# Optimization experiments

Hardware: AMD Instinct MI355X
Metric: run time of the kernel (lower is better)

The kernel has to match this reference:

```python
import jax, jax.numpy as jnp
import numpy as np

NUM_HEADS = 16
EPS = 1e-5


def _layernorm(x, w):
    # torch LayerNorm (biased variance), bias=False
    m = jnp.mean(x, axis=-1, keepdims=True)
    v = jnp.mean(jnp.square(x - m), axis=-1, keepdims=True)
    return (x - m) * jax.lax.rsqrt(v + EPS) * w


def setup_inputs() -> dict:
    key = jax.random.key(0)
    ks = jax.random.split(key, 8)
    B, S, H, A = 2, 2048, 1024, 1024
    hd = H // NUM_HEADS
    return {
        "x": jax.random.normal(ks[0], (B, S, H), jnp.float32),
        "ada_cond": jax.random.normal(ks[1], (B, A), jnp.float32),
        "freqs": jax.random.normal(ks[2], (S, hd // 2, 2), jnp.float32),
        "w_qkv": jax.random.normal(ks[3], (3 * H, H), jnp.float32) * (1.0 / np.sqrt(H)),
        "w_o": jax.random.normal(ks[4], (H, H), jnp.float32) * (1.0 / np.sqrt(H)),
        "ln_w": jnp.ones((H,), jnp.float32),
        "mod_w": jax.random.normal(ks[5], (3 * H, A), jnp.float32) * 0.02,
        "mod_b": jax.random.normal(ks[6], (3 * H,), jnp.float32) * 0.02,
        "qn_w": jnp.ones((hd,), jnp.float32),
        "kn_w": jnp.ones((hd,), jnp.float32),
    }


def reference(x, ada_cond, freqs, w_qkv, w_o, ln_w, mod_w, mod_b, qn_w, kn_w):
    B, S, H = x.shape
    nh = NUM_HEADS
    hd = H // nh

    # pre-norm + AdaLN modulation (with gate)
    h = _layernorm(x, ln_w)
    mod = (jax.nn.silu(ada_cond) @ mod_w.T + mod_b)[:, None, :]  # [B,1,3H]
    scale, shift, gate = jnp.split(mod, 3, axis=-1)
    h = h * (scale + 1.0) + shift

    # QKV projection and head split
    qkv = h @ w_qkv.T                                  # [B,S,3H]
    q, k, v = jnp.split(qkv, 3, axis=-1)
    to_heads = lambda t: t.reshape(B, S, nh, hd).transpose(0, 2, 1, 3)  # [B,nh,S,hd]
    q, k, v = to_heads(q), to_heads(k), to_heads(v)

    # per-head QK layernorm
    q = _layernorm(q, qn_w)
    k = _layernorm(k, kn_w)

    # RoPE (complex rotation via interleaved pairs)
    f = freqs[:S].reshape(1, 1, S, hd // 2, 2)

    def rope(t):
        tr = t.reshape(B, nh, S, hd // 2, 2)
        re = tr[..., 0] * f[..., 0] - tr[..., 1] * f[..., 1]
        im = tr[..., 1] * f[..., 0] + tr[..., 0] * f[..., 1]
        return jnp.stack([re, im], axis=-1).reshape(B, nh, S, hd)

    q, k = rope(q), rope(k)

    # scaled dot-product attention (non-causal)
    scores = jnp.einsum("bhqd,bhkd->bhqk", q, k) * (1.0 / np.sqrt(hd))
    attn = jax.nn.softmax(scores, axis=-1)
    o = jnp.einsum("bhqk,bhkd->bhqd", attn, v)
    o = o.transpose(0, 2, 1, 3).reshape(B, S, H)

    return (o @ w_o.T) * gate
```

## Files before the change

### kernel.cpp

```cpp
#include <hip/hip_runtime.h>
#include <hip/hip_bf16.h>
#include <hip/hip_fp16.h>
#include <math.h>

#define B_ 2
#define S_ 2048
#define H_ 1024
#define A_ 1024
#define NH_ 16
#define HD_ 64
#define H3_ 3072
#define EPS_ 1e-5f

typedef __attribute__((ext_vector_type(8))) short short8;
typedef __attribute__((ext_vector_type(4))) float floatx4;
typedef __attribute__((ext_vector_type(4))) _Float16 half4v;
typedef __attribute__((ext_vector_type(2))) __fp16 fp16x2;

__device__ inline unsigned short f2bf(float x) {
    union { float f; unsigned u; } v; v.f = x;
    unsigned r = v.u + 0x7fffu + ((v.u >> 16) & 1u);
    return (unsigned short)(r >> 16);
}

__device__ inline unsigned pk_bf16(float a, float b) {
    union { __hip_bfloat162 h; unsigned u; } v;
    v.h = __float22bfloat162_rn(make_float2(a, b));
    return v.u;
}

__device__ inline unsigned pk_f16(float a, float b) {
    union { __half2 h; unsigned u; } v;
    v.h = __float22half2_rn(make_float2(a, b));
    return v.u;
}

__device__ inline void gld_lds16(const void* g, void* l) {
    __builtin_amdgcn_global_load_lds(
        (const __attribute__((address_space(1))) unsigned int*)g,
        (__attribute__((address_space(3))) unsigned int*)l, 16, 0, 0);
}


__global__ __launch_bounds__(256) void cast_bf16_kernel(
    const float* __restrict__ in, unsigned short* __restrict__ out, int n)
{
    int i = (blockIdx.x * 256 + threadIdx.x) * 8;
    if (i >= n) return;
    float4 a = *(const float4*)(in + i);
    float4 b = *(const float4*)(in + i + 4);
    uint4 o;
    o.x = pk_bf16(a.x, a.y);
    o.y = pk_bf16(a.z, a.w);
    o.z = pk_bf16(b.x, b.y);
    o.w = pk_bf16(b.z, b.w);
    *(uint4*)(out + i) = o;
}

__global__ __launch_bounds__(256) void mod_gemv_kernel(
    const float* __restrict__ ada, const float* __restrict__ mod_w,
    const float* __restrict__ mod_b, float* __restrict__ mod)
{
    int wid = threadIdx.x >> 6;
    int lane = threadIdx.x & 63;
    int idx = blockIdx.x * 4 + wid;
    int b = idx / H3_;
    int j = idx % H3_;
    const float* ar = ada + (size_t)b * A_;
    const float* wr = mod_w + (size_t)j * A_;
    float acc = 0.f;
    for (int a = lane; a < A_; a += 64) {
        float av = ar[a];
        float sv = av / (1.f + __expf(-av));
        acc += sv * wr[a];
    }
    #pragma unroll
    for (int m = 1; m < 64; m <<= 1) acc += __shfl_xor(acc, m);
    if (lane == 0) mod[idx] = acc + mod_b[j];
}

__global__ __launch_bounds__(256) void ln_mod_kernel(
    const float* __restrict__ x, const float* __restrict__ ln_w,
    const float* __restrict__ mod, unsigned short* __restrict__ hout)
{
    int row = blockIdx.x;
    int b = row >> 11;
    const float* xr = x + (size_t)row * H_;
    int t = threadIdx.x;
    float4 xv = *(const float4*)(xr + t * 4);
    float s1 = xv.x + xv.y + xv.z + xv.w;
    float s2 = xv.x*xv.x + xv.y*xv.y + xv.z*xv.z + xv.w*xv.w;
    #pragma unroll
    for (int m = 1; m < 64; m <<= 1) { s1 += __shfl_xor(s1, m); s2 += __shfl_xor(s2, m); }
    __shared__ float r1[4], r2[4];
    int wid = t >> 6, lane = t & 63;
    if (lane == 0) { r1[wid] = s1; r2[wid] = s2; }
    __syncthreads();
    s1 = r1[0] + r1[1] + r1[2] + r1[3];
    s2 = r2[0] + r2[1] + r2[2] + r2[3];
    float mean = s1 * (1.f / H_);
    float var  = s2 * (1.f / H_) - mean * mean;
    float rstd = rsqrtf(var + EPS_);
    const float* mrow = mod + (size_t)b * H3_;
    float4 wv = *(const float4*)(ln_w + t * 4);
    float4 sc = *(const float4*)(mrow + t * 4);
    float4 sh = *(const float4*)(mrow + H_ + t * 4);
    float4 hv;
    hv.x = (xv.x - mean) * rstd * wv.x * (sc.x + 1.f) + sh.x;
    hv.y = (xv.y - mean) * rstd * wv.y * (sc.y + 1.f) + sh.y;
    hv.z = (xv.z - mean) * rstd * wv.z * (sc.z + 1.f) + sh.z;
    hv.w = (xv.w - mean) * rstd * wv.w * (sc.w + 1.f) + sh.w;
    uint2 o;
    o.x = pk_bf16(hv.x, hv.y);
    o.y = pk_bf16(hv.z, hv.w);
    *(uint2*)(hout + (size_t)row * H_ + t * 4) = o;
}

__global__ __launch_bounds__(256) void gemm_qkv_fused_kernel(
    const unsigned short* __restrict__ A, const unsigned short* __restrict__ Bm,
    const float* __restrict__ freqs, const float* __restrict__ qn_w,
    const float* __restrict__ kn_w, unsigned short* __restrict__ qout,
    unsigned short* __restrict__ kout, unsigned short* __restrict__ vtout)
{
    __shared__ unsigned short As[2][128 * 32];
    __shared__ unsigned short Bs[2][128 * 32];
    const int K = H_;
    int t = threadIdx.x;
    int w = t >> 6, lane = t & 63;
    int q16 = lane & 15, quad = lane >> 4;
    int wm = w >> 1, wn = w & 1;
    int m0 = blockIdx.y * 128, n0 = blockIdx.x * 128;

    int srow = 2 * (lane >> 3) + ((lane >> 2) & 1);
    int scol = ((lane & 3) ^ ((lane >> 3) & 3)) << 3;
    const unsigned short* ga = A + (size_t)(m0 + (w << 5) + srow) * K + scol;
    const unsigned short* gb = Bm + (size_t)(n0 + (w << 5) + srow) * K + scol;
    int ldst0 = (w * 16) * 64;
    int ldst1 = (w * 16 + 8) * 64;

    floatx4 acc[4][4];
    #pragma unroll
    for (int mt = 0; mt < 4; ++mt)
        #pragma unroll
        for (int nt = 0; nt < 4; ++nt)
            acc[mt][nt] = (floatx4){0.f, 0.f, 0.f, 0.f};

    int abase = (wm * 32 + (q16 >> 1)) * 64 + (q16 & 1) * 32
              + ((quad ^ ((q16 >> 1) & 3)) << 3);
    int bbase = (wn * 32 + (q16 >> 1)) * 64 + (q16 & 1) * 32
              + ((quad ^ ((q16 >> 1) & 3)) << 3);

    gld_lds16(ga, &As[0][ldst0]);
    gld_lds16(ga + (size_t)16 * K, &As[0][ldst1]);
    gld_lds16(gb, &Bs[0][ldst0]);
    gld_lds16(gb + (size_t)16 * K, &Bs[0][ldst1]);
    __syncthreads();

    int cur = 0;
    for (int kt = 0; kt < K / 32; ++kt) {
        const unsigned short* curA = &As[cur][0];
        const unsigned short* curB = &Bs[cur][0];
        short8 af[4], bf[4];
        #pragma unroll
        for (int mt = 0; mt < 4; ++mt)
            af[mt] = *(const short8*)&curA[abase + mt * 512];
        #pragma unroll
        for (int nt = 0; nt < 4; ++nt)
            bf[nt] = *(const short8*)&curB[bbase + nt * 512];

        if (kt + 1 < K / 32) {
            const unsigned short* ga2 = ga + (kt + 1) * 32;
            const unsigned short* gb2 = gb + (kt + 1) * 32;
            int nb = cur ^ 1;
            gld_lds16(ga2, &As[nb][ldst0]);
            gld_lds16(ga2 + (size_t)16 * K, &As[nb][ldst1]);
            gld_lds16(gb2, &Bs[nb][ldst0]);
            gld_lds16(gb2 + (size_t)16 * K, &Bs[nb][ldst1]);
        }

        #pragma unroll
        for (int mt = 0; mt < 4; ++mt)
            #pragma unroll
            for (int nt = 0; nt < 4; ++nt)
                acc[mt][nt] = __builtin_amdgcn_mfma_f32_16x16x32_bf16(
                    af[mt], bf[nt], acc[mt][nt], 0, 0, 0);

        __syncthreads();
        cur ^= 1;
    }

    int n_base = n0 + wn * 64;
    int sec = n_base >> 10;
    int head = (n_base & 1023) >> 6;

    if (sec == 2) {
        #pragma unroll
        for (int mt = 0; mt < 4; ++mt) {
            int m = m0 + wm * 64 + mt * 16 + quad * 4;
            int b = m >> 11, s = m & (S_ - 1);
            #pragma unroll
            for (int nt = 0; nt < 4; ++nt) {
                int d = nt * 16 + q16;
                unsigned short* dst =
                    vtout + ((size_t)((b * 16 + head) * 64 + d)) * S_ + s;
                uint2 pk;
                pk.x = pk_f16(acc[mt][nt][0], acc[mt][nt][1]);
                pk.y = pk_f16(acc[mt][nt][2], acc[mt][nt][3]);
                *(uint2*)dst = pk;
            }
        }
    } else {
        const float* nw = (sec == 0) ? qn_w : kn_w;
        float w4[4];
        #pragma unroll
        for (int nt = 0; nt < 4; ++nt) w4[nt] = nw[nt * 16 + q16];
        unsigned short* outp = (sec == 0) ? qout : kout;
        float qscale = (sec == 0) ? 0.1803368801111244f : 1.0f;

        #pragma unroll
        for (int mt = 0; mt < 4; ++mt) {
            #pragma unroll
            for (int i = 0; i < 4; ++i) {
                int m = m0 + wm * 64 + mt * 16 + quad * 4 + i;
                int b = m >> 11, s = m & (S_ - 1);
                float v0 = acc[mt][0][i], v1 = acc[mt][1][i];
                float v2 = acc[mt][2][i], v3 = acc[mt][3][i];
                float s1 = (v0 + v1) + (v2 + v3);
                float s2 = (v0 * v0 + v1 * v1) + (v2 * v2 + v3 * v3);
                #pragma unroll
                for (int msk = 1; msk < 16; msk <<= 1) {
                    s1 += __shfl_xor(s1, msk);
                    s2 += __shfl_xor(s2, msk);
                }
                float mean = s1 * (1.f / 64);
                float var  = s2 * (1.f / 64) - mean * mean;
                float rstd = rsqrtf(var + EPS_);
                float vv[4];
                vv[0] = (v0 - mean) * rstd * w4[0];
                vv[1] = (v1 - mean) * rstd * w4[1];
                vv[2] = (v2 - mean) * rstd * w4[2];
                vv[3] = (v3 - mean) * rstd * w4[3];
                const float* fr = freqs + (size_t)s * 64;
                unsigned short* orow = outp + ((size_t)((b * 16 + head) * S_ + s)) * 64;
                #pragma unroll
                for (int nt = 0; nt < 4; ++nt) {
                    int c = nt * 16 + q16;
                    float vp = __shfl_xor(vv[nt], 1);
                    float2 ff = *(const float2*)(fr + (c & ~1));
                    float r = (c & 1) ? (vv[nt] * ff.x + vp * ff.y)
                                      : (vv[nt] * ff.x - vp * ff.y);
                    orow[c] = f2bf(r * qscale);
                }
            }
        }
    }
}

__global__ __launch_bounds__(256) void gemm_bt_bf16_kernel(
    const unsigned short* __restrict__ A, const unsigned short* __restrict__ Bm,
    float* __restrict__ C, int M, int N, int K,
    const float* __restrict__ gate, int gate_stride, int batch_shift)
{
    __shared__ unsigned short As[2][128 * 32];
    __shared__ unsigned short Bs[2][64 * 32];
    int t = threadIdx.x;
    int w = t >> 6, lane = t & 63;
    int q16 = lane & 15, quad = lane >> 4;
    int m0 = blockIdx.y * 128, n0 = blockIdx.x * 64;

    int srow = 2 * (lane >> 3) + ((lane >> 2) & 1);
    int scol = ((lane & 3) ^ ((lane >> 3) & 3)) << 3;
    const unsigned short* ga = A + (size_t)(m0 + (w << 5) + srow) * K + scol;
    const unsigned short* gb = Bm + (size_t)(n0 + (w << 4) + srow) * K + scol;
    int ldstA0 = (w * 16) * 64;
    int ldstA1 = (w * 16 + 8) * 64;
    int ldstB  = (w * 8) * 64;

    floatx4 acc[2][4];
    #pragma unroll
    for (int mt = 0; mt < 2; ++mt)
        #pragma unroll
        for (int nt = 0; nt < 4; ++nt)
            acc[mt][nt] = (floatx4){0.f, 0.f, 0.f, 0.f};

    int abase = (w * 16 + (q16 >> 1)) * 64 + (q16 & 1) * 32
              + ((quad ^ ((q16 >> 1) & 3)) << 3);
    int bbase = (q16 >> 1) * 64 + (q16 & 1) * 32
              + ((quad ^ ((q16 >> 1) & 3)) << 3);

    gld_lds16(ga, &As[0][ldstA0]);
    gld_lds16(ga + (size_t)16 * K, &As[0][ldstA1]);
    gld_lds16(gb, &Bs[0][ldstB]);
    __syncthreads();

    int cur = 0;
    for (int kt = 0; kt < K / 32; ++kt) {
        const unsigned short* curA = &As[cur][0];
        const unsigned short* curB = &Bs[cur][0];
        short8 af[2], bf[4];
        #pragma unroll
        for (int mt = 0; mt < 2; ++mt)
            af[mt] = *(const short8*)&curA[abase + mt * 512];
        #pragma unroll
        for (int nt = 0; nt < 4; ++nt)
            bf[nt] = *(const short8*)&curB[bbase + nt * 512];

        if (kt + 1 < K / 32) {
            const unsigned short* ga2 = ga + (kt + 1) * 32;
            const unsigned short* gb2 = gb + (kt + 1) * 32;
            int nb = cur ^ 1;
            gld_lds16(ga2, &As[nb][ldstA0]);
            gld_lds16(ga2 + (size_t)16 * K, &As[nb][ldstA1]);
            gld_lds16(gb2, &Bs[nb][ldstB]);
        }

        #pragma unroll
        for (int mt = 0; mt < 2; ++mt)
            #pragma unroll
            for (int nt = 0; nt < 4; ++nt)
                acc[mt][nt] = __builtin_amdgcn_mfma_f32_16x16x32_bf16(
                    af[mt], bf[nt], acc[mt][nt], 0, 0, 0);

        __syncthreads();
        cur ^= 1;
    }

    #pragma unroll
    for (int mt = 0; mt < 2; ++mt) {
        #pragma unroll
        for (int i = 0; i < 4; ++i) {
            int m = m0 + w * 32 + mt * 16 + quad * 4 + i;
            float* crow = C + (size_t)m * N;
            const float* grow = gate ? gate + (size_t)(m >> batch_shift) * gate_stride
                                     : nullptr;
            #pragma unroll
            for (int nt = 0; nt < 4; ++nt) {
                int n = n0 + nt * 16 + q16;
                float v = acc[mt][nt][i];
                if (gate) v *= grow[n];
                crow[n] = v;
            }
        }
    }
}

__global__ __launch_bounds__(256, 2) void attn_mfma_kernel(
    const unsigned short* __restrict__ q, const unsigned short* __restrict__ k,
    const unsigned short* __restrict__ vt, unsigned short* __restrict__ o)
{
    __shared__ __align__(16) float obuf[4096];
    __shared__ float lbuf[4][4][16];

    int t = threadIdx.x;
    int w = t >> 6, lane = t & 63;
    int q16 = lane & 15, quad = lane >> 4;
    int bh = blockIdx.y, b = bh >> 4, h = bh & 15;
    int s0 = blockIdx.x * 64;

    const unsigned short* qgp = q + ((size_t)bh * S_ + s0) * HD_;
    short8 qf[4][2];
    #pragma unroll
    for (int qg = 0; qg < 4; ++qg)
        #pragma unroll
        for (int hh = 0; hh < 2; ++hh)
            qf[qg][hh] = *(const short8*)(qgp + (16 * qg + q16) * HD_ + hh * 32 + quad * 8);

    const unsigned short* kg = k + (size_t)bh * S_ * HD_ + (16 * w + q16) * HD_ + quad * 8;
    const unsigned short* vg = vt + (size_t)bh * 64 * S_ + (size_t)q16 * S_
                             + 16 * w + quad * 4;

    short8 kf_nx0 = *(const short8*)kg;
    short8 kf_nx1 = *(const short8*)(kg + 32);
    half4v vf_nx[4];
    #pragma unroll
    for (int nd = 0; nd < 4; ++nd)
        vf_nx[nd] = *(const half4v*)(vg + nd * 16 * S_);

    union { half4v h; uint2 u; } ones;
    ones.u.x = 0x3C003C00u; ones.u.y = 0x3C003C00u;

    floatx4 acc_o[4][4];
    floatx4 acc_l[4];
    #pragma unroll
    for (int nd = 0; nd < 4; ++nd)
        #pragma unroll
        for (int qg = 0; qg < 4; ++qg)
            acc_o[nd][qg] = (floatx4){0.f, 0.f, 0.f, 0.f};
    #pragma unroll
    for (int qg = 0; qg < 4; ++qg) acc_l[qg] = (floatx4){0.f, 0.f, 0.f, 0.f};

    for (int kt = 0; kt < S_ / 64; ++kt) {
        short8 kf0 = kf_nx0, kf1 = kf_nx1;
        half4v vf0 = vf_nx[0], vf1 = vf_nx[1], vf2 = vf_nx[2], vf3 = vf_nx[3];

        if (kt + 1 < S_ / 64) {
            kg += 64 * HD_; vg += 64;
            kf_nx0 = *(const short8*)kg;
            kf_nx1 = *(const short8*)(kg + 32);
            #pragma unroll
            for (int nd = 0; nd < 4; ++nd)
                vf_nx[nd] = *(const half4v*)(vg + nd * 16 * S_);
        }

        floatx4 sc[4];
        #pragma unroll
        for (int qg = 0; qg < 4; ++qg) sc[qg] = (floatx4){-12.f, -12.f, -12.f, -12.f};
        #pragma unroll
        for (int qg = 0; qg < 4; ++qg) {
            sc[qg] = __builtin_amdgcn_mfma_f32_16x16x32_bf16(kf0, qf[qg][0], sc[qg], 0, 0, 0);
            sc[qg] = __builtin_amdgcn_mfma_f32_16x16x32_bf16(kf1, qf[qg][1], sc[qg], 0, 0, 0);
        }

        #pragma unroll
        for (int qg = 0; qg < 4; ++qg) {
            float p0 = __builtin_amdgcn_exp2f(sc[qg][0]);
            float p1 = __builtin_amdgcn_exp2f(sc[qg][1]);
            float p2 = __builtin_amdgcn_exp2f(sc[qg][2]);
            float p3 = __builtin_amdgcn_exp2f(sc[qg][3]);
            union { half4v h; fp16x2 f2[2]; } pf;
            pf.f2[0] = __builtin_amdgcn_cvt_pkrtz(p0, p1);
            pf.f2[1] = __builtin_amdgcn_cvt_pkrtz(p2, p3);
            acc_l[qg] = __builtin_amdgcn_mfma_f32_16x16x16f16(ones.h, pf.h, acc_l[qg], 0, 0, 0);
            acc_o[0][qg] = __builtin_amdgcn_mfma_f32_16x16x16f16(vf0, pf.h, acc_o[0][qg], 0, 0, 0);
            acc_o[1][qg] = __builtin_amdgcn_mfma_f32_16x16x16f16(vf1, pf.h, acc_o[1][qg], 0, 0, 0);
            acc_o[2][qg] = __builtin_amdgcn_mfma_f32_16x16x16f16(vf2, pf.h, acc_o[2][qg], 0, 0, 0);
            acc_o[3][qg] = __builtin_amdgcn_mfma_f32_16x16x16f16(vf3, pf.h, acc_o[3][qg], 0, 0, 0);
        }
    }

    if (quad == 0) {
        #pragma unroll
        for (int qg = 0; qg < 4; ++qg) lbuf[w][qg][q16] = acc_l[qg][0];
    }
    __syncthreads();
    float linv = 1.f / (lbuf[0][w][q16] + lbuf[1][w][q16] + lbuf[2][w][q16] + lbuf[3][w][q16]);

    float* myw = obuf + ((w * 4) * 64 + lane) * 4;
    float* myr = obuf + (w * 64 + lane) * 4;
    unsigned short* og = o + ((size_t)(b * S_ + s0 + 16 * w + q16)) * H_ + h * HD_ + 4 * quad;

    #pragma unroll
    for (int nd = 0; nd < 4; ++nd) {
        __syncthreads();
        #pragma unroll
        for (int qg = 0; qg < 4; ++qg)
            *(floatx4*)(myw + qg * 256) = acc_o[nd][qg];
        __syncthreads();
        floatx4 r0 = *(const floatx4*)(myr);
        floatx4 r1 = *(const floatx4*)(myr + 1024);
        floatx4 r2 = *(const floatx4*)(myr + 2048);
        floatx4 r3 = *(const floatx4*)(myr + 3072);
        floatx4 s = (r0 + r1) + (r2 + r3);
        uint2 pk;
        pk.x = pk_bf16(s[0] * linv, s[1] * linv);
        pk.y = pk_bf16(s[2] * linv, s[3] * linv);
        *(uint2*)(og + nd * 16) = pk;
    }
}

extern "C" void kernel_launch(void* const* d_in, const int* in_sizes, int n_in,
                              void* d_out, int out_size, void* d_ws, size_t ws_size,
                              hipStream_t stream)
{
    const float* x     = (const float*)d_in[0];
    const float* ada   = (const float*)d_in[1];
    const float* freqs = (const float*)d_in[2];
    const float* w_qkv = (const float*)d_in[3];
    const float* w_o   = (const float*)d_in[4];
    const float* ln_w  = (const float*)d_in[5];
    const float* mod_w = (const float*)d_in[6];
    const float* mod_b = (const float*)d_in[7];
    const float* qn_w  = (const float*)d_in[8];
    const float* kn_w  = (const float*)d_in[9];
    float* out = (float*)d_out;

    float* ws  = (float*)d_ws;
    float* mod = ws;
    unsigned short* hb    = (unsigned short*)(mod + 8192);
    unsigned short* qb    = hb + (size_t)B_ * S_ * H_;
    unsigned short* kb    = qb + (size_t)B_ * S_ * H_;
    unsigned short* vtb   = kb + (size_t)B_ * S_ * H_;
    unsigned short* ob    = vtb + (size_t)B_ * S_ * H_;
    unsigned short* wqkvb = ob + (size_t)B_ * S_ * H_;
    unsigned short* wob   = wqkvb + (size_t)H3_ * H_;

    cast_bf16_kernel<<<H3_ * H_ / (8 * 256), 256, 0, stream>>>(w_qkv, wqkvb, H3_ * H_);
    cast_bf16_kernel<<<H_ * H_ / (8 * 256), 256, 0, stream>>>(w_o, wob, H_ * H_);
    mod_gemv_kernel<<<B_ * H3_ / 4, 256, 0, stream>>>(ada, mod_w, mod_b, mod);
    ln_mod_kernel<<<B_ * S_, 256, 0, stream>>>(x, ln_w, mod, hb);
    gemm_qkv_fused_kernel<<<dim3(H3_ / 128, B_ * S_ / 128), 256, 0, stream>>>(
        hb, wqkvb, freqs, qn_w, kn_w, qb, kb, vtb);
    attn_mfma_kernel<<<dim3(S_ / 64, B_ * NH_), 256, 0, stream>>>(qb, kb, vtb, ob);
    gemm_bt_bf16_kernel<<<dim3(H_ / 64, B_ * S_ / 128), 256, 0, stream>>>(
        ob, wob, out, B_ * S_, H_, H_, mod + 2 * H_, H3_, 11);
}
```

Baseline: 286.2 us.

## Stage V tiles through double-buffered swizzled LDS in attention kernel

The attention kernel used to load V fragments straight from global memory in 8-byte pieces strided by sequence rows. It now does coalesced 16-byte loads of each V tile into a double-buffered, XOR-swizzled LDS buffer, prefetching one tile ahead in registers, and each wave then reads its MFMA operands from LDS. This is meant to cut uncoalesced global traffic for V. In exchange it adds a __syncthreads per key tile and uses 16KB of LDS, which is reused for the output reduction.

```diff
diff --git a/kernel.cpp b/kernel.cpp
--- a/kernel.cpp
+++ b/kernel.cpp
@@ -40,7 +40,6 @@
         (const __attribute__((address_space(1))) unsigned int*)g,
         (__attribute__((address_space(3))) unsigned int*)l, 16, 0, 0);
 }
-
 
 __global__ __launch_bounds__(256) void cast_bf16_kernel(
     const float* __restrict__ in, unsigned short* __restrict__ out, int n)
@@ -348,8 +347,9 @@
     const unsigned short* __restrict__ q, const unsigned short* __restrict__ k,
     const unsigned short* __restrict__ vt, unsigned short* __restrict__ o)
 {
-    __shared__ __align__(16) float obuf[4096];
+    __shared__ __align__(16) unsigned char smem[16 * 1024];
     __shared__ float lbuf[4][4][16];
+    unsigned short* Vs = (unsigned short*)smem;
 
     int t = threadIdx.x;
     int w = t >> 6, lane = t & 63;
@@ -366,15 +366,28 @@
             qf[qg][hh] = *(const short8*)(qgp + (16 * qg + q16) * HD_ + hh * 32 + quad * 8);
 
     const unsigned short* kg = k + (size_t)bh * S_ * HD_ + (16 * w + q16) * HD_ + quad * 8;
-    const unsigned short* vg = vt + (size_t)bh * 64 * S_ + (size_t)q16 * S_
-                             + 16 * w + quad * 4;
+
+    const unsigned short* vg0 = vt + (size_t)bh * 64 * S_
+                              + (size_t)(16 * w + (lane >> 3)) * S_ + (lane & 7) * 8;
+    const unsigned short* vg1 = vg0 + 8 * S_;
+    unsigned short* vw0 = Vs + (16 * w + (lane >> 3)) * 64 + (((lane & 7) ^ (lane >> 3)) << 3);
+    unsigned short* vw1 = vw0 + 512;
+    int vroff = q16 * 64 + (((2 * w + (quad >> 1)) ^ (q16 & 7)) << 3) + ((quad & 1) << 2);
+
+    const int NT = S_ / 64;
 
     short8 kf_nx0 = *(const short8*)kg;
     short8 kf_nx1 = *(const short8*)(kg + 32);
-    half4v vf_nx[4];
-    #pragma unroll
-    for (int nd = 0; nd < 4; ++nd)
-        vf_nx[nd] = *(const half4v*)(vg + nd * 16 * S_);
+    uint4 vr0 = *(const uint4*)vg0;
+    uint4 vr1 = *(const uint4*)vg1;
+    vg0 += 64; vg1 += 64;
+
+    *(uint4*)vw0 = vr0;
+    *(uint4*)vw1 = vr1;
+    vr0 = *(const uint4*)vg0;
+    vr1 = *(const uint4*)vg1;
+    vg0 += 64; vg1 += 64;
+    __syncthreads();
 
     union { half4v h; uint2 u; } ones;
     ones.u.x = 0x3C003C00u; ones.u.y = 0x3C003C00u;
@@ -389,17 +402,22 @@
     #pragma unroll
     for (int qg = 0; qg < 4; ++qg) acc_l[qg] = (floatx4){0.f, 0.f, 0.f, 0.f};
 
-    for (int kt = 0; kt < S_ / 64; ++kt) {
+    int cur = 0;
+    for (int kt = 0; kt < NT; ++kt) {
         short8 kf0 = kf_nx0, kf1 = kf_nx1;
-        half4v vf0 = vf_nx[0], vf1 = vf_nx[1], vf2 = vf_nx[2], vf3 = vf_nx[3];
-
-        if (kt + 1 < S_ / 64) {
-            kg += 64 * HD_; vg += 64;
+
+        if (kt + 1 < NT) {
+            int nb = cur ^ 1;
+            *(uint4*)(vw0 + nb * 4096) = vr0;
+            *(uint4*)(vw1 + nb * 4096) = vr1;
+            kg += 64 * HD_;
             kf_nx0 = *(const short8*)kg;
             kf_nx1 = *(const short8*)(kg + 32);
-            #pragma unroll
-            for (int nd = 0; nd < 4; ++nd)
-                vf_nx[nd] = *(const half4v*)(vg + nd * 16 * S_);
+            if (kt + 2 < NT) {
+                vr0 = *(const uint4*)vg0;
+                vr1 = *(const uint4*)vg1;
+                vg0 += 64; vg1 += 64;
+            }
         }
 
         floatx4 sc[4];
@@ -410,6 +428,12 @@
             sc[qg] = __builtin_amdgcn_mfma_f32_16x16x32_bf16(kf0, qf[qg][0], sc[qg], 0, 0, 0);
             sc[qg] = __builtin_amdgcn_mfma_f32_16x16x32_bf16(kf1, qf[qg][1], sc[qg], 0, 0, 0);
         }
+
+        const unsigned short* vbase = Vs + cur * 4096;
+        half4v vf[4];
+        #pragma unroll
+        for (int nd = 0; nd < 4; ++nd)
+            vf[nd] = *(const half4v*)&vbase[vroff + nd * 1024];
 
         #pragma unroll
         for (int qg = 0; qg < 4; ++qg) {
@@ -421,11 +445,14 @@
             pf.f2[0] = __builtin_amdgcn_cvt_pkrtz(p0, p1);
             pf.f2[1] = __builtin_amdgcn_cvt_pkrtz(p2, p3);
             acc_l[qg] = __builtin_amdgcn_mfma_f32_16x16x16f16(ones.h, pf.h, acc_l[qg], 0, 0, 0);
-            acc_o[0][qg] = __builtin_amdgcn_mfma_f32_16x16x16f16(vf0, pf.h, acc_o[0][qg], 0, 0, 0);
-            acc_o[1][qg] = __builtin_amdgcn_mfma_f32_16x16x16f16(vf1, pf.h, acc_o[1][qg], 0, 0, 0);
-            acc_o[2][qg] = __builtin_amdgcn_mfma_f32_16x16x16f16(vf2, pf.h, acc_o[2][qg], 0, 0, 0);
-            acc_o[3][qg] = __builtin_amdgcn_mfma_f32_16x16x16f16(vf3, pf.h, acc_o[3][qg], 0, 0, 0);
-        }
+            #pragma unroll
+            for (int nd = 0; nd < 4; ++nd)
+                acc_o[nd][qg] = __builtin_amdgcn_mfma_f32_16x16x16f16(
+                    vf[nd], pf.h, acc_o[nd][qg], 0, 0, 0);
+        }
+
+        __syncthreads();
+        cur ^= 1;
     }
 
     if (quad == 0) {
@@ -435,6 +462,7 @@
     __syncthreads();
     float linv = 1.f / (lbuf[0][w][q16] + lbuf[1][w][q16] + lbuf[2][w][q16] + lbuf[3][w][q16]);
 
+    float* obuf = (float*)smem;
     float* myw = obuf + ((w * 4) * 64 + lane) * 4;
     float* myr = obuf + (w * 64 + lane) * 4;
     unsigned short* og = o + ((size_t)(b * S_ + s0 + 16 * w + q16)) * H_ + h * HD_ + 4 * quad;
```

Result: faster. 253.6 us (-11.4%).
